# Kernel tuning notes

Hardware: AMD Instinct MI355X
Metric: run time of the kernel (lower is better)

Reference implementation:

```python
import jax, jax.numpy as jnp
import numpy as np

B, N, D, FUSE, A = 512, 1024, 1024, 1024, 256


def setup_inputs() -> dict:
    key = jax.random.key(0)
    ks = jax.random.split(key, 6)
    return {
        "confounder_set": jax.random.normal(ks[0], (N, D), dtype=jnp.float32),
        "fuse_rep": jax.random.normal(ks[1], (B, FUSE), dtype=jnp.float32),
        "probabilities": jax.random.uniform(ks[2], (1, N), dtype=jnp.float32),
        "Wq": jax.random.normal(ks[3], (FUSE, A), dtype=jnp.float32) / np.sqrt(FUSE),
        "Wk": jax.random.normal(ks[4], (D, A), dtype=jnp.float32) / np.sqrt(D),
        "wt": jax.random.normal(ks[5], (A,), dtype=jnp.float32) / np.sqrt(A),
    }


def reference(confounder_set, fuse_rep, probabilities, Wq, Wk, wt):
    # query: [B, A], key: [N, A]
    q = fuse_rep @ Wq
    k = confounder_set @ Wk
    # broadcasted add + tanh -> [B, N, A]
    fuse = jnp.tanh(q[:, None, :] + k[None, :, :])
    # scoring linear -> [B, N]
    scores = jnp.einsum("bna,a->bn", fuse, wt)
    attn = jax.nn.softmax(scores, axis=1)           # [B, N]
    probs = probabilities[0]                        # [N]  (transpose(0,1) of [1,N])
    # probability-weighted confounder sum -> [B, D]
    fin = jnp.einsum("bn,nd->bd", attn * probs[None, :], confounder_set)
    return fin
```

## Files before the change

### kernel.cpp

```cpp
#include <hip/hip_runtime.h>
#include <hip/hip_bf16.h>

#define B 512
#define N 1024
#define D 1024
#define FUSE 1024
#define A 256

typedef float f32x4 __attribute__((ext_vector_type(4)));
typedef short bf16x8 __attribute__((ext_vector_type(8)));
typedef unsigned short u16x4 __attribute__((ext_vector_type(4)));

__device__ __forceinline__ float fast_exp2(float x) { return __builtin_amdgcn_exp2f(x); }
__device__ __forceinline__ float fast_rcp(float x)  { return __builtin_amdgcn_rcpf(x); }

static constexpr float TANH_C = 2.8853900817779268f;
static constexpr float LOG2E  = 1.4426950408889634f;

__device__ __forceinline__ unsigned short f2bf(float x) {
    __hip_bfloat16 h = __float2bfloat16(x);
    return *reinterpret_cast<unsigned short*>(&h);
}

__global__ __launch_bounds__(256) void cast_kernel(
    const float* __restrict__ fuse, const float* __restrict__ conf,
    const float* __restrict__ Wq, const float* __restrict__ Wk,
    short* __restrict__ fuse_bf, short* __restrict__ conf_bf,
    short* __restrict__ confT, short* __restrict__ WqT, short* __restrict__ WkT)
{
    __shared__ float tile[64 * 65];
    int bid = blockIdx.x;
    const float* src; short* dstS = nullptr; short* dstT = nullptr;
    int r0, c0, spitch; float scale = 1.0f;
    if (bid < 128) {
        src = fuse; dstS = fuse_bf; spitch = FUSE;
        r0 = (bid >> 4) * 64; c0 = (bid & 15) * 64;
    } else if (bid < 384) {
        int b = bid - 128; src = conf; dstS = conf_bf; dstT = confT; spitch = D;
        r0 = (b >> 4) * 64; c0 = (b & 15) * 64;
    } else if (bid < 448) {
        int b = bid - 384; src = Wq; dstT = WqT; spitch = A; scale = TANH_C;
        r0 = (b >> 2) * 64; c0 = (b & 3) * 64;
    } else {
        int b = bid - 448; src = Wk; dstT = WkT; spitch = A; scale = TANH_C;
        r0 = (b >> 2) * 64; c0 = (b & 3) * 64;
    }
    const int tr = threadIdx.x >> 4, tc = (threadIdx.x & 15) * 4;

    f32x4 v[4];
#pragma unroll
    for (int i = 0; i < 4; ++i) {
        v[i] = *(const f32x4*)(src + (size_t)(r0 + tr + 16 * i) * spitch + c0 + tc);
#pragma unroll
        for (int j = 0; j < 4; ++j) v[i][j] *= scale;
    }
    if (dstS) {
#pragma unroll
        for (int i = 0; i < 4; ++i) {
            u16x4 o;
#pragma unroll
            for (int j = 0; j < 4; ++j) o[j] = f2bf(v[i][j]);
            *(u16x4*)(dstS + (size_t)(r0 + tr + 16 * i) * spitch + c0 + tc) = o;
        }
    }
    if (dstT) {
#pragma unroll
        for (int i = 0; i < 4; ++i)
#pragma unroll
            for (int j = 0; j < 4; ++j) tile[(tr + 16 * i) * 65 + tc + j] = v[i][j];
        __syncthreads();
#pragma unroll
        for (int i = 0; i < 4; ++i) {
            int orow = tr + 16 * i;
            u16x4 o;
#pragma unroll
            for (int j = 0; j < 4; ++j) o[j] = f2bf(tile[(tc + j) * 65 + orow]);
            *(u16x4*)(dstT + (size_t)(c0 + orow) * 1024 + r0 + tc) = o;
        }
    }
}

__device__ __forceinline__ void gemm32x64_pipe(
    const short* __restrict__ Ag, const short* __restrict__ Btg,
    float* __restrict__ C, int ldc, int m0, int n0,
    char* As, char* Bs)
{
    const int tid = threadIdx.x;
    const int w = tid >> 6, l = tid & 63;
    const int wm = w >> 1, wn = w & 1;
    const int lr = l & 15;
    const int cr = (l >> 4) * 4;
    const int rsub = l >> 3;
    const int ssrc = ((l & 7) ^ rsub) << 3;

    auto stage = [&](int buf, int k0) {
        {
            int row = (w << 3) | rsub;
            __builtin_amdgcn_global_load_lds(
                (const __attribute__((address_space(1))) unsigned int*)
                    (Ag + (size_t)(m0 + row) * 1024 + k0 + ssrc),
                (__attribute__((address_space(3))) unsigned int*)(As + (buf << 12) + (w << 10)),
                16, 0, 0);
        }
#pragma unroll
        for (int p = 0; p < 2; ++p) {
            int chunk = (w << 1) | p;
            int row = (chunk << 3) | rsub;
            __builtin_amdgcn_global_load_lds(
                (const __attribute__((address_space(1))) unsigned int*)
                    (Btg + (size_t)(n0 + row) * 1024 + k0 + ssrc),
                (__attribute__((address_space(3))) unsigned int*)(Bs + (buf << 13) + (chunk << 10)),
                16, 0, 0);
        }
    };

    f32x4 acc[2] = {};
    stage(0, 0);
    asm volatile("s_waitcnt vmcnt(0)" ::: "memory");
    __builtin_amdgcn_s_barrier();

    int cur = 0;
    for (int t = 0; t < 16; ++t) {
        if (t < 15) stage(cur ^ 1, (t + 1) << 6);

        const char* Ab = As + (cur << 12);
        const char* Bb = Bs + (cur << 13);
#pragma unroll
        for (int ks = 0; ks < 2; ++ks) {
            int j = ks * 64 + ((l >> 4) << 4);
            int r = wm * 16 + lr;
            bf16x8 af = *(const bf16x8*)(Ab + r * 128 + (j ^ ((r & 7) << 4)));
#pragma unroll
            for (int i = 0; i < 2; ++i) {
                int c = wn * 32 + i * 16 + lr;
                bf16x8 bq = *(const bf16x8*)(Bb + c * 128 + (j ^ ((c & 7) << 4)));
                acc[i] = __builtin_amdgcn_mfma_f32_16x16x32_bf16(af, bq, acc[i], 0, 0, 0);
            }
        }
        asm volatile("s_waitcnt vmcnt(0)" ::: "memory");
        __builtin_amdgcn_s_barrier();
        cur ^= 1;
    }

#pragma unroll
    for (int i = 0; i < 2; ++i) {
        float* cp = C + (size_t)(m0 + wm * 16 + cr) * ldc + n0 + wn * 32 + i * 16 + lr;
#pragma unroll
        for (int r = 0; r < 4; ++r) cp[(size_t)r * ldc] = acc[i][r];
    }
}

__global__ __launch_bounds__(256) void qk_gemm_kernel(
    const short* __restrict__ fuse_bf, const short* __restrict__ conf_bf,
    const short* __restrict__ WqT, const short* __restrict__ WkT,
    float* __restrict__ qbuf, float* __restrict__ kbuf)
{
    __shared__ char As[8192];
    __shared__ char Bs[16384];
    int bid = blockIdx.x;
    if (bid < 64) {
        gemm32x64_pipe(fuse_bf, WqT, qbuf, A, (bid >> 2) * 32, (bid & 3) * 64, As, Bs);
    } else {
        bid -= 64;
        gemm32x64_pipe(conf_bf, WkT, kbuf, A, (bid >> 2) * 32, (bid & 3) * 64, As, Bs);
    }
}

__global__ __launch_bounds__(256) void fin_gemm_kernel(
    const short* __restrict__ wb, const short* __restrict__ confT,
    float* __restrict__ out)
{
    __shared__ char As[8192];
    __shared__ char Bs[16384];
    gemm32x64_pipe(wb, confT, out, D, blockIdx.y * 32, blockIdx.x * 64, As, Bs);
}

__global__ __launch_bounds__(256) void scores_kernel(
    const float* __restrict__ qbuf, const float* __restrict__ kbuf,
    const float* __restrict__ wt, float* __restrict__ sbuf)
{
    __shared__ f32x4 qs[32 * 32];
    __shared__ f32x4 ks[64 * 32];
    const int tid = threadIdx.x;
    const int bid = blockIdx.x;
    const int b0 = (bid & 15) * 32;
    const int n0 = (bid >> 4) * 64;

    const f32x4* q4 = (const f32x4*)qbuf;
    const f32x4* k4 = (const f32x4*)kbuf;
    const f32x4* wt4 = (const f32x4*)wt;
    const int bl = tid >> 5;
    const int nl = tid & 31;

    float a00 = 0.f, a10 = 0.f, a20 = 0.f, a30 = 0.f;
    float a01 = 0.f, a11 = 0.f, a21 = 0.f, a31 = 0.f;
#pragma unroll
    for (int c = 0; c < 2; ++c) {
#pragma unroll
        for (int j = 0; j < 4; ++j) {
            int idx = tid + j * 256;
            int r = idx >> 5, col = idx & 31;
            qs[r * 32 + col] = q4[(size_t)(b0 + r) * 64 + c * 32 + col];
        }
#pragma unroll
        for (int j = 0; j < 8; ++j) {
            int idx = tid + j * 256;
            int r = idx >> 5, col = idx & 31;
            ks[r * 32 + (col ^ (r & 15))] = k4[(size_t)(n0 + r) * 64 + c * 32 + col];
        }
        __syncthreads();
        for (int a4 = 0; a4 < 32; ++a4) {
            int kx = a4 ^ (nl & 15);
            f32x4 kv0 = ks[nl * 32 + kx];
            f32x4 kv1 = ks[(nl + 32) * 32 + kx];
            f32x4 wv = wt4[c * 32 + a4];
            f32x4 q0 = qs[(bl) * 32 + a4];
            f32x4 q1 = qs[(bl + 8) * 32 + a4];
            f32x4 q2 = qs[(bl + 16) * 32 + a4];
            f32x4 q3 = qs[(bl + 24) * 32 + a4];
#pragma unroll
            for (int cc = 0; cc < 4; ++cc) {
                float k0 = kv0[cc], k1 = kv1[cc], wc = wv[cc];
                a00 += wc * fast_rcp(fast_exp2(q0[cc] + k0) + 1.0f);
                a10 += wc * fast_rcp(fast_exp2(q1[cc] + k0) + 1.0f);
                a20 += wc * fast_rcp(fast_exp2(q2[cc] + k0) + 1.0f);
                a30 += wc * fast_rcp(fast_exp2(q3[cc] + k0) + 1.0f);
                a01 += wc * fast_rcp(fast_exp2(q0[cc] + k1) + 1.0f);
                a11 += wc * fast_rcp(fast_exp2(q1[cc] + k1) + 1.0f);
                a21 += wc * fast_rcp(fast_exp2(q2[cc] + k1) + 1.0f);
                a31 += wc * fast_rcp(fast_exp2(q3[cc] + k1) + 1.0f);
            }
        }
        __syncthreads();
    }
    sbuf[(size_t)(b0 + bl) * N + n0 + nl]           = -2.0f * a00;
    sbuf[(size_t)(b0 + bl + 8) * N + n0 + nl]       = -2.0f * a10;
    sbuf[(size_t)(b0 + bl + 16) * N + n0 + nl]      = -2.0f * a20;
    sbuf[(size_t)(b0 + bl + 24) * N + n0 + nl]      = -2.0f * a30;
    sbuf[(size_t)(b0 + bl) * N + n0 + 32 + nl]      = -2.0f * a01;
    sbuf[(size_t)(b0 + bl + 8) * N + n0 + 32 + nl]  = -2.0f * a11;
    sbuf[(size_t)(b0 + bl + 16) * N + n0 + 32 + nl] = -2.0f * a21;
    sbuf[(size_t)(b0 + bl + 24) * N + n0 + 32 + nl] = -2.0f * a31;
}

__global__ __launch_bounds__(256) void softmax_kernel(
    const float* __restrict__ s, const float* __restrict__ probs,
    short* __restrict__ wbuf)
{
    const int b = blockIdx.x, tid = threadIdx.x;
    const f32x4* s4 = (const f32x4*)(s + (size_t)b * N);
    f32x4 v = s4[tid];

    f32x4 e;
#pragma unroll
    for (int c = 0; c < 4; ++c) e[c] = fast_exp2(v[c] * LOG2E);
    float sum = e[0] + e[1] + e[2] + e[3];
    for (int off = 32; off > 0; off >>= 1) sum += __shfl_xor(sum, off);
    __shared__ float reds[4];
    const int wid = tid >> 6, lane = tid & 63;
    if (lane == 0) reds[wid] = sum;
    __syncthreads();
    sum = reds[0] + reds[1] + reds[2] + reds[3];

    const float inv = fast_rcp(sum);
    const f32x4* p4 = (const f32x4*)probs;
    f32x4 p = p4[tid];
    u16x4 o;
#pragma unroll
    for (int c = 0; c < 4; ++c) o[c] = f2bf(e[c] * inv * p[c]);
    ((u16x4*)(wbuf + (size_t)b * N))[tid] = o;
}

extern "C" void kernel_launch(void* const* d_in, const int* in_sizes, int n_in,
                              void* d_out, int out_size, void* d_ws, size_t ws_size,
                              hipStream_t stream) {
    const float* conf     = (const float*)d_in[0];
    const float* fuse_rep = (const float*)d_in[1];
    const float* probs    = (const float*)d_in[2];
    const float* Wq       = (const float*)d_in[3];
    const float* Wk       = (const float*)d_in[4];
    const float* wt       = (const float*)d_in[5];
    float* out = (float*)d_out;

    char* w = (char*)d_ws;
    float* qbuf   = (float*)(w);
    float* kbuf   = (float*)(w + (1u << 20));
    float* sbuf   = (float*)(w + (3u << 20));
    short* fuse_bf= (short*)(w + (5u << 20));
    short* conf_bf= (short*)(w + (6u << 20));
    short* confT  = (short*)(w + (8u << 20));
    short* WqT    = (short*)(w + (10u << 20));
    short* WkT    = (short*)(w + (10u << 20) + (512u << 10));
    short* wbuf   = (short*)(w);

    hipLaunchKernelGGL(cast_kernel, dim3(512), dim3(256), 0, stream,
                       fuse_rep, conf, Wq, Wk, fuse_bf, conf_bf, confT, WqT, WkT);
    hipLaunchKernelGGL(qk_gemm_kernel, dim3(192), dim3(256), 0, stream,
                       fuse_bf, conf_bf, WqT, WkT, qbuf, kbuf);
    hipLaunchKernelGGL(scores_kernel, dim3(256), dim3(256), 0, stream,
                       qbuf, kbuf, wt, sbuf);
    hipLaunchKernelGGL(softmax_kernel, dim3(B), dim3(256), 0, stream,
                       sbuf, probs, wbuf);
    hipLaunchKernelGGL(fin_gemm_kernel, dim3(D / 64, B / 32), dim3(256), 0, stream,
                       wbuf, confT, out);
}
```

Measured before the change: 135.8 us.

## Fuse softmax into scores kernel with atomic row sums and deferred normalization

Removes the separate softmax kernel. The scores kernel now exponentiates its scores directly, writes unnormalized prob-weighted bf16 weights, and accumulates per-row sums with atomics. The final GEMM scales its output rows by the reciprocal of those sums. The scores tile is halved to 32x32 per block, which doubles the grid and reduces register pressure. There is no max subtraction, which relies on scores being bounded (|score| ≤ sum|wt|), and the float atomics make the row sums nondeterministic.

```diff
diff --git a/kernel.cpp b/kernel.cpp
--- a/kernel.cpp
+++ b/kernel.cpp
@@ -14,8 +14,8 @@
 __device__ __forceinline__ float fast_exp2(float x) { return __builtin_amdgcn_exp2f(x); }
 __device__ __forceinline__ float fast_rcp(float x)  { return __builtin_amdgcn_rcpf(x); }
 
-static constexpr float TANH_C = 2.8853900817779268f;
-static constexpr float LOG2E  = 1.4426950408889634f;
+static constexpr float TANH_C     = 2.8853900817779268f;
+static constexpr float NEG2LOG2E  = -2.8853900817779268f;
 
 __device__ __forceinline__ unsigned short f2bf(float x) {
     __hip_bfloat16 h = __float2bfloat16(x);
@@ -26,10 +26,14 @@
     const float* __restrict__ fuse, const float* __restrict__ conf,
     const float* __restrict__ Wq, const float* __restrict__ Wk,
     short* __restrict__ fuse_bf, short* __restrict__ conf_bf,
-    short* __restrict__ confT, short* __restrict__ WqT, short* __restrict__ WkT)
+    short* __restrict__ confT, short* __restrict__ WqT, short* __restrict__ WkT,
+    float* __restrict__ rowsum)
 {
     __shared__ float tile[64 * 65];
     int bid = blockIdx.x;
+    if (bid == 0 && threadIdx.x < 128)
+        ((f32x4*)rowsum)[threadIdx.x] = f32x4{0.f, 0.f, 0.f, 0.f};
+
     const float* src; short* dstS = nullptr; short* dstT = nullptr;
     int r0, c0, spitch; float scale = 1.0f;
     if (bid < 128) {
@@ -80,9 +84,11 @@
     }
 }
 
+template <bool SCALE_ROWS>
 __device__ __forceinline__ void gemm32x64_pipe(
     const short* __restrict__ Ag, const short* __restrict__ Btg,
     float* __restrict__ C, int ldc, int m0, int n0,
+    const float* __restrict__ rowsum,
     char* As, char* Bs)
 {
     const int tid = threadIdx.x;
@@ -142,11 +148,17 @@
         cur ^= 1;
     }
 
+    f32x4 inv = {1.f, 1.f, 1.f, 1.f};
+    if (SCALE_ROWS) {
+        const f32x4 rs = *(const f32x4*)(rowsum + m0 + wm * 16 + cr);
+#pragma unroll
+        for (int r = 0; r < 4; ++r) inv[r] = fast_rcp(rs[r]);
+    }
 #pragma unroll
     for (int i = 0; i < 2; ++i) {
         float* cp = C + (size_t)(m0 + wm * 16 + cr) * ldc + n0 + wn * 32 + i * 16 + lr;
 #pragma unroll
-        for (int r = 0; r < 4; ++r) cp[(size_t)r * ldc] = acc[i][r];
+        for (int r = 0; r < 4; ++r) cp[(size_t)r * ldc] = acc[i][r] * inv[r];
     }
 }
 
@@ -159,32 +171,36 @@
     __shared__ char Bs[16384];
     int bid = blockIdx.x;
     if (bid < 64) {
-        gemm32x64_pipe(fuse_bf, WqT, qbuf, A, (bid >> 2) * 32, (bid & 3) * 64, As, Bs);
+        gemm32x64_pipe<false>(fuse_bf, WqT, qbuf, A, (bid >> 2) * 32, (bid & 3) * 64,
+                              nullptr, As, Bs);
     } else {
         bid -= 64;
-        gemm32x64_pipe(conf_bf, WkT, kbuf, A, (bid >> 2) * 32, (bid & 3) * 64, As, Bs);
+        gemm32x64_pipe<false>(conf_bf, WkT, kbuf, A, (bid >> 2) * 32, (bid & 3) * 64,
+                              nullptr, As, Bs);
     }
 }
 
 __global__ __launch_bounds__(256) void fin_gemm_kernel(
     const short* __restrict__ wb, const short* __restrict__ confT,
-    float* __restrict__ out)
+    const float* __restrict__ rowsum, float* __restrict__ out)
 {
     __shared__ char As[8192];
     __shared__ char Bs[16384];
-    gemm32x64_pipe(wb, confT, out, D, blockIdx.y * 32, blockIdx.x * 64, As, Bs);
+    gemm32x64_pipe<true>(wb, confT, out, D, blockIdx.y * 32, blockIdx.x * 64,
+                         rowsum, As, Bs);
 }
 
 __global__ __launch_bounds__(256) void scores_kernel(
     const float* __restrict__ qbuf, const float* __restrict__ kbuf,
-    const float* __restrict__ wt, float* __restrict__ sbuf)
+    const float* __restrict__ wt, const float* __restrict__ probs,
+    short* __restrict__ wbuf, float* __restrict__ rowsum)
 {
     __shared__ f32x4 qs[32 * 32];
-    __shared__ f32x4 ks[64 * 32];
+    __shared__ f32x4 ks[32 * 32];
     const int tid = threadIdx.x;
     const int bid = blockIdx.x;
     const int b0 = (bid & 15) * 32;
-    const int n0 = (bid >> 4) * 64;
+    const int n0 = (bid >> 4) * 32;
 
     const f32x4* q4 = (const f32x4*)qbuf;
     const f32x4* k4 = (const f32x4*)kbuf;
@@ -192,8 +208,7 @@
     const int bl = tid >> 5;
     const int nl = tid & 31;
 
-    float a00 = 0.f, a10 = 0.f, a20 = 0.f, a30 = 0.f;
-    float a01 = 0.f, a11 = 0.f, a21 = 0.f, a31 = 0.f;
+    float acc0 = 0.f, acc1 = 0.f, acc2 = 0.f, acc3 = 0.f;
 #pragma unroll
     for (int c = 0; c < 2; ++c) {
 #pragma unroll
@@ -201,18 +216,11 @@
             int idx = tid + j * 256;
             int r = idx >> 5, col = idx & 31;
             qs[r * 32 + col] = q4[(size_t)(b0 + r) * 64 + c * 32 + col];
-        }
-#pragma unroll
-        for (int j = 0; j < 8; ++j) {
-            int idx = tid + j * 256;
-            int r = idx >> 5, col = idx & 31;
             ks[r * 32 + (col ^ (r & 15))] = k4[(size_t)(n0 + r) * 64 + c * 32 + col];
         }
         __syncthreads();
         for (int a4 = 0; a4 < 32; ++a4) {
-            int kx = a4 ^ (nl & 15);
-            f32x4 kv0 = ks[nl * 32 + kx];
-            f32x4 kv1 = ks[(nl + 32) * 32 + kx];
+            f32x4 kv = ks[nl * 32 + (a4 ^ (nl & 15))];
             f32x4 wv = wt4[c * 32 + a4];
             f32x4 q0 = qs[(bl) * 32 + a4];
             f32x4 q1 = qs[(bl + 8) * 32 + a4];
@@ -220,55 +228,41 @@
             f32x4 q3 = qs[(bl + 24) * 32 + a4];
 #pragma unroll
             for (int cc = 0; cc < 4; ++cc) {
-                float k0 = kv0[cc], k1 = kv1[cc], wc = wv[cc];
-                a00 += wc * fast_rcp(fast_exp2(q0[cc] + k0) + 1.0f);
-                a10 += wc * fast_rcp(fast_exp2(q1[cc] + k0) + 1.0f);
-                a20 += wc * fast_rcp(fast_exp2(q2[cc] + k0) + 1.0f);
-                a30 += wc * fast_rcp(fast_exp2(q3[cc] + k0) + 1.0f);
-                a01 += wc * fast_rcp(fast_exp2(q0[cc] + k1) + 1.0f);
-                a11 += wc * fast_rcp(fast_exp2(q1[cc] + k1) + 1.0f);
-                a21 += wc * fast_rcp(fast_exp2(q2[cc] + k1) + 1.0f);
-                a31 += wc * fast_rcp(fast_exp2(q3[cc] + k1) + 1.0f);
+                float kc = kv[cc], wc = wv[cc];
+                acc0 += wc * fast_rcp(fast_exp2(q0[cc] + kc) + 1.0f);
+                acc1 += wc * fast_rcp(fast_exp2(q1[cc] + kc) + 1.0f);
+                acc2 += wc * fast_rcp(fast_exp2(q2[cc] + kc) + 1.0f);
+                acc3 += wc * fast_rcp(fast_exp2(q3[cc] + kc) + 1.0f);
             }
         }
         __syncthreads();
     }
-    sbuf[(size_t)(b0 + bl) * N + n0 + nl]           = -2.0f * a00;
-    sbuf[(size_t)(b0 + bl + 8) * N + n0 + nl]       = -2.0f * a10;
-    sbuf[(size_t)(b0 + bl + 16) * N + n0 + nl]      = -2.0f * a20;
-    sbuf[(size_t)(b0 + bl + 24) * N + n0 + nl]      = -2.0f * a30;
-    sbuf[(size_t)(b0 + bl) * N + n0 + 32 + nl]      = -2.0f * a01;
-    sbuf[(size_t)(b0 + bl + 8) * N + n0 + 32 + nl]  = -2.0f * a11;
-    sbuf[(size_t)(b0 + bl + 16) * N + n0 + 32 + nl] = -2.0f * a21;
-    sbuf[(size_t)(b0 + bl + 24) * N + n0 + 32 + nl] = -2.0f * a31;
-}
-
-__global__ __launch_bounds__(256) void softmax_kernel(
-    const float* __restrict__ s, const float* __restrict__ probs,
-    short* __restrict__ wbuf)
-{
-    const int b = blockIdx.x, tid = threadIdx.x;
-    const f32x4* s4 = (const f32x4*)(s + (size_t)b * N);
-    f32x4 v = s4[tid];
-
-    f32x4 e;
-#pragma unroll
-    for (int c = 0; c < 4; ++c) e[c] = fast_exp2(v[c] * LOG2E);
-    float sum = e[0] + e[1] + e[2] + e[3];
-    for (int off = 32; off > 0; off >>= 1) sum += __shfl_xor(sum, off);
-    __shared__ float reds[4];
-    const int wid = tid >> 6, lane = tid & 63;
-    if (lane == 0) reds[wid] = sum;
-    __syncthreads();
-    sum = reds[0] + reds[1] + reds[2] + reds[3];
-
-    const float inv = fast_rcp(sum);
-    const f32x4* p4 = (const f32x4*)probs;
-    f32x4 p = p4[tid];
-    u16x4 o;
-#pragma unroll
-    for (int c = 0; c < 4; ++c) o[c] = f2bf(e[c] * inv * p[c]);
-    ((u16x4*)(wbuf + (size_t)b * N))[tid] = o;
+
+    const float e0 = fast_exp2(acc0 * NEG2LOG2E);
+    const float e1 = fast_exp2(acc1 * NEG2LOG2E);
+    const float e2 = fast_exp2(acc2 * NEG2LOG2E);
+    const float e3 = fast_exp2(acc3 * NEG2LOG2E);
+
+    const float pcol = probs[n0 + nl];
+    wbuf[(size_t)(b0 + bl) * N + n0 + nl]      = (short)f2bf(e0 * pcol);
+    wbuf[(size_t)(b0 + bl + 8) * N + n0 + nl]  = (short)f2bf(e1 * pcol);
+    wbuf[(size_t)(b0 + bl + 16) * N + n0 + nl] = (short)f2bf(e2 * pcol);
+    wbuf[(size_t)(b0 + bl + 24) * N + n0 + nl] = (short)f2bf(e3 * pcol);
+
+    float s0 = e0, s1 = e1, s2 = e2, s3 = e3;
+#pragma unroll
+    for (int off = 16; off > 0; off >>= 1) {
+        s0 += __shfl_xor(s0, off);
+        s1 += __shfl_xor(s1, off);
+        s2 += __shfl_xor(s2, off);
+        s3 += __shfl_xor(s3, off);
+    }
+    if (nl == 0) {
+        atomicAdd(rowsum + b0 + bl,      s0);
+        atomicAdd(rowsum + b0 + bl + 8,  s1);
+        atomicAdd(rowsum + b0 + bl + 16, s2);
+        atomicAdd(rowsum + b0 + bl + 24, s3);
+    }
 }
 
 extern "C" void kernel_launch(void* const* d_in, const int* in_sizes, int n_in,
@@ -285,22 +279,21 @@
     char* w = (char*)d_ws;
     float* qbuf   = (float*)(w);
     float* kbuf   = (float*)(w + (1u << 20));
-    float* sbuf   = (float*)(w + (3u << 20));
-    short* fuse_bf= (short*)(w + (5u << 20));
-    short* conf_bf= (short*)(w + (6u << 20));
-    short* confT  = (short*)(w + (8u << 20));
-    short* WqT    = (short*)(w + (10u << 20));
-    short* WkT    = (short*)(w + (10u << 20) + (512u << 10));
-    short* wbuf   = (short*)(w);
+    short* wbuf   = (short*)(w + (2u << 20));
+    float* rowsum = (float*)(w + (3u << 20));
+    short* fuse_bf= (short*)(w + (4u << 20));
+    short* conf_bf= (short*)(w + (5u << 20));
+    short* confT  = (short*)(w + (7u << 20));
+    short* WqT    = (short*)(w + (9u << 20));
+    short* WkT    = (short*)(w + (9u << 20) + (512u << 10));
 
     hipLaunchKernelGGL(cast_kernel, dim3(512), dim3(256), 0, stream,
-                       fuse_rep, conf, Wq, Wk, fuse_bf, conf_bf, confT, WqT, WkT);
+                       fuse_rep, conf, Wq, Wk, fuse_bf, conf_bf, confT, WqT, WkT,
+                       rowsum);
     hipLaunchKernelGGL(qk_gemm_kernel, dim3(192), dim3(256), 0, stream,
                        fuse_bf, conf_bf, WqT, WkT, qbuf, kbuf);
-    hipLaunchKernelGGL(scores_kernel, dim3(256), dim3(256), 0, stream,
-                       qbuf, kbuf, wt, sbuf);
-    hipLaunchKernelGGL(softmax_kernel, dim3(B), dim3(256), 0, stream,
-                       sbuf, probs, wbuf);
+    hipLaunchKernelGGL(scores_kernel, dim3(512), dim3(256), 0, stream,
+                       qbuf, kbuf, wt, probs, wbuf, rowsum);
     hipLaunchKernelGGL(fin_gemm_kernel, dim3(D / 64, B / 32), dim3(256), 0, stream,
-                       wbuf, confT, out);
-}
+                       wbuf, confT, rowsum, out);
+}
```

Measured after the change: 133.6 us. About the same (-1.6%).
